# Kernel tuning notes

Measured on AMD Instinct MI355X. Metric: run time of the kernel, lower is better.

The kernel has to match this reference:

```python
import jax, jax.numpy as jnp
import numpy as np
from jax import lax

CONTEXT = 7
EPS = 1e-5  # BatchNorm2d default eps
DN = ('NCHW', 'OIHW', 'NCHW')


def _cbr(x, W, b, g, be, m, v, padding):
    # conv2d + BatchNorm (eval, running stats) + ReLU
    y = lax.conv_general_dilated(x, W, (1, 1), padding, dimension_numbers=DN)
    y = y + b[None, :, None, None]
    y = (y - m[None, :, None, None]) * (g / jnp.sqrt(v + EPS))[None, :, None, None] + be[None, :, None, None]
    return jax.nn.relu(y)


def _pool21(x):  # MaxPool2d(kernel_size=(2,1))
    return lax.reduce_window(x, -jnp.inf, lax.max, (1, 1, 2, 1), (1, 1, 2, 1), 'VALID')


def setup_inputs() -> dict:
    key = jax.random.key(0)
    ks = jax.random.split(key, 16)
    B, T, F, NC = 16, 108, 144, 25
    d = {}
    d['x'] = jax.random.normal(ks[0], (B, T, F), jnp.float32)
    d['labels'] = jax.random.randint(ks[1], (B, T), 0, NC)
    shapes = [(32, 1, 3, 3), (32, 32, 3, 3), (32, 32, 3, 3), (32, 32, 3, 3),
              (64, 32, 3, 3), (64, 64, 3, 3), (128, 64, 12, 9)]
    for i, s in enumerate(shapes, 1):
        fan_in = s[1] * s[2] * s[3]
        d[f'W{i}'] = jax.random.normal(ks[1 + i], s, jnp.float32) / np.sqrt(fan_in).astype(np.float32)
        c = s[0]
        d[f'b{i}'] = jnp.zeros((c,), jnp.float32)
        d[f'g{i}'] = jnp.ones((c,), jnp.float32)
        d[f'be{i}'] = jnp.zeros((c,), jnp.float32)
        d[f'm{i}'] = jnp.zeros((c,), jnp.float32)
        d[f'v{i}'] = jnp.ones((c,), jnp.float32)
    d['W8'] = jax.random.normal(ks[9], (NC, 128, 1, 1), jnp.float32) / np.float32(np.sqrt(128.0))
    d['b8'] = jnp.zeros((NC,), jnp.float32)
    return d


def reference(x, labels,
              W1, b1, g1, be1, m1, v1,
              W2, b2, g2, be2, m2, v2,
              W3, b3, g3, be3, m3, v3,
              W4, b4, g4, be4, m4, v4,
              W5, b5, g5, be5, m5, v5,
              W6, b6, g6, be6, m6, v6,
              W7, b7, g7, be7, m7, v7,
              W8, b8):
    B, T, F = x.shape
    win_len = 2 * CONTEXT + 1
    # permute to [B, F, T], zero-pad time by CONTEXT on both sides
    xp = jnp.pad(jnp.transpose(x, (0, 2, 1)), ((0, 0), (0, 0), (CONTEXT, CONTEXT)))
    # vectorized sliding windows (replaces the nested python loop of slices+cat)
    idx = jnp.arange(T)[:, None] + jnp.arange(win_len)[None, :]  # [T, 15]
    win = xp[:, :, idx]                                          # [B, F, T, 15]
    h = jnp.transpose(win, (0, 2, 1, 3)).reshape(B * T, 1, F, win_len)
    h = _cbr(h, W1, b1, g1, be1, m1, v1, 'SAME')
    h = _cbr(h, W2, b2, g2, be2, m2, v2, 'SAME')
    h = _cbr(h, W3, b3, g3, be3, m3, v3, 'SAME')
    h = _cbr(h, W4, b4, g4, be4, m4, v4, 'SAME')
    h = _pool21(h)  # dropout2d is identity in eval
    h = _cbr(h, W5, b5, g5, be5, m5, v5, 'VALID')
    h = _cbr(h, W6, b6, g6, be6, m6, v6, 'VALID')
    h = _pool21(h)
    h = _cbr(h, W7, b7, g7, be7, m7, v7, 'VALID')
    h = lax.conv_general_dilated(h, W8, (1, 1), 'VALID', dimension_numbers=DN) + b8[None, :, None, None]
    logits = jnp.mean(h, axis=(2, 3))  # AvgPool2d over full spatial extent
    return logits.reshape(B, T, -1)    # probs_out=True -> CRF input
```

## Files before the change

kernel.cpp:

```cpp
#include <hip/hip_runtime.h>
#include <hip/hip_bf16.h>
#include <hip/hip_fp16.h>

#define REGH 93440
#define C6N 26112

typedef _Float16 v8h __attribute__((ext_vector_type(8)));
typedef float v4f __attribute__((ext_vector_type(4)));
typedef unsigned short u16x8 __attribute__((ext_vector_type(8)));

__device__ inline float h2f(unsigned short u) {
    union { unsigned short s; _Float16 h; } v; v.s = u; return (float)v.h;
}
__device__ inline unsigned short f2h(float f) {
    union { unsigned short s; _Float16 h; } v; v.h = (_Float16)f; return v.s;
}

__global__ void repack_k(const float* __restrict__ W, const float* __restrict__ bb,
                         const float* __restrict__ gg, const float* __restrict__ be,
                         const float* __restrict__ mm, const float* __restrict__ vv,
                         float* __restrict__ wOut, float* __restrict__ tOut,
                         int CIN, int KHW, int COUT)
{
    int gid = blockIdx.x * 256 + threadIdx.x;
    if (gid < COUT) {
        float s = gg[gid] * rsqrtf(vv[gid] + 1e-5f);
        tOut[gid] = (bb[gid] - mm[gid]) * s + be[gid];
    }
    int tot = CIN * KHW * COUT;
    if (gid >= tot) return;
    int co = gid % COUT;
    int rest = gid / COUT;
    int k = rest % KHW;
    int ci = rest / KHW;
    float s = gg[co] * rsqrtf(vv[co] + 1e-5f);
    wOut[gid] = W[(co * CIN + ci) * KHW + k] * s;
}

__global__ void repack_mfma_k(const float* __restrict__ W, const float* __restrict__ bb,
                              const float* __restrict__ gg, const float* __restrict__ be,
                              const float* __restrict__ mm, const float* __restrict__ vv,
                              unsigned short* __restrict__ frag, float* __restrict__ tOut,
                              int CIN, int NT, int HALVES)
{
    int gid = blockIdx.x * 256 + threadIdx.x;
    int COUT = NT * 16;
    if (gid < COUT) {
        float s = gg[gid] * rsqrtf(vv[gid] + 1e-5f);
        tOut[gid] = (bb[gid] - mm[gid]) * s + be[gid];
    }
    int tot = 9 * HALVES * NT * 512;
    if (gid >= tot) return;
    int j    = gid & 7;
    int lane = (gid >> 3) & 63;
    int nt   = (gid >> 9) % NT;
    int rest = (gid >> 9) / NT;
    int half = rest % HALVES;
    int khw  = rest / HALVES;
    int ci   = half * 32 + (lane >> 4) * 8 + j;
    int co   = nt * 16 + (lane & 15);
    int kh   = khw / 3, kw = khw % 3;
    float s = gg[co] * rsqrtf(vv[co] + 1e-5f);
    frag[gid] = f2h(W[((co * CIN + ci) * 3 + kh) * 3 + kw] * s);
}

__global__ void repack7_k(const float* __restrict__ W, const float* __restrict__ bb,
                          const float* __restrict__ gg, const float* __restrict__ be,
                          const float* __restrict__ mm, const float* __restrict__ vv,
                          unsigned short* __restrict__ frag, float* __restrict__ tOut)
{
    int gid = blockIdx.x * 256 + threadIdx.x;
    if (gid < 128) {
        float s = gg[gid] * rsqrtf(vv[gid] + 1e-5f);
        tOut[gid] = (bb[gid] - mm[gid]) * s + be[gid];
    }
    if (gid >= 884736) return;
    int j    = gid & 7;
    int lane = (gid >> 3) & 63;
    int nt   = (gid >> 9) & 7;
    int half = (gid >> 12) & 1;
    int khw  = gid >> 13;
    int co   = nt * 16 + (lane & 15);
    int ci   = half * 32 + (lane >> 4) * 8 + j;
    int kh   = khw / 9, kw = khw - kh * 9;
    float s = gg[co] * rsqrtf(vv[co] + 1e-5f);
    frag[gid] = f2h(W[((co * 64 + ci) * 12 + kh) * 9 + kw] * s);
}

__global__ void zero_rings_k(unsigned short* __restrict__ bufA,
                             unsigned short* __restrict__ bufB, int cn)
{
    int gid = blockIdx.x * 256 + threadIdx.x;
    int tot = cn * 2 * 4 * 328;
    if (gid >= tot) return;
    int e = gid % 328;
    int rest = gid / 328;
    int cg = rest % 4; rest /= 4;
    int bsel = rest & 1;
    int nl = rest >> 1;
    unsigned short* base = (bsel ? bufB : bufA) + (size_t)nl * REGH + cg * 23360;
    int row, col;
    if (e < 40) { row = (e < 20) ? 0 : 145; col = (e < 20) ? e : e - 20; }
    else { int e2 = e - 40; row = 1 + (e2 >> 1); col = (e2 & 1) ? 16 : 0; }
    *(u16x8*)(base + (row * 20 + col) * 8) = (u16x8){0,0,0,0,0,0,0,0};
}

__global__ __launch_bounds__(256) void conv1_k(
    const float* __restrict__ x, unsigned short* __restrict__ out,
    const float* __restrict__ wr, const float* __restrict__ tv,
    int c0, int cn)
{
    int gid = blockIdx.x * 256 + threadIdx.x;
    if (gid >= cn * 2160) return;
    int nl = gid / 2160, p = gid - nl * 2160;
    int f = p / 15, w = p - f * 15;
    int n = c0 + nl;
    int b = n / 108, t = n - b * 108;

    float acc[32];
#pragma unroll
    for (int i = 0; i < 32; ++i) acc[i] = 0.f;

    for (int kh = 0; kh < 3; ++kh) {
        int ff = f + kh - 1;
        if (ff < 0 || ff >= 144) continue;
        for (int kw = 0; kw < 3; ++kw) {
            int c = w + kw - 1;
            if (c < 0 || c >= 15) continue;
            int tt = t + c - 7;
            if (tt < 0 || tt >= 108) continue;
            float xval = x[(b * 108 + tt) * 144 + ff];
            const float* wp = wr + (kh * 3 + kw) * 32;
#pragma unroll
            for (int q = 0; q < 8; ++q) {
                float4 wv = *(const float4*)(wp + q * 4);
                acc[q * 4 + 0] = fmaf(xval, wv.x, acc[q * 4 + 0]);
                acc[q * 4 + 1] = fmaf(xval, wv.y, acc[q * 4 + 1]);
                acc[q * 4 + 2] = fmaf(xval, wv.z, acc[q * 4 + 2]);
                acc[q * 4 + 3] = fmaf(xval, wv.w, acc[q * 4 + 3]);
            }
        }
    }
    unsigned short* ob = out + (size_t)nl * REGH + ((f + 1) * 20 + (w + 1)) * 8;
#pragma unroll
    for (int cg = 0; cg < 4; ++cg) {
        u16x8 pk;
#pragma unroll
        for (int c = 0; c < 8; ++c)
            pk[c] = f2h(fmaxf(acc[cg * 8 + c] + tv[cg * 8 + c], 0.f));
        *(u16x8*)(ob + cg * 23360) = pk;
    }
}

template<bool POOL>
__global__ __launch_bounds__(256) void conv234m_k(
    const unsigned short* __restrict__ in, unsigned short* __restrict__ out,
    const unsigned short* __restrict__ frag, const float* __restrict__ tv)
{
    __shared__ __align__(16) unsigned short sA[11552];
    const int band = blockIdx.x;
    const int n = blockIdx.y;
    const int tid = threadIdx.x;
    const int wave = tid >> 6, lane = tid & 63;
    const int m = lane & 15, quad = lane >> 4;

    {
        const float4* src = (const float4*)(in + (size_t)n * REGH);
        float4* dst = (float4*)sA;
        for (int i = tid; i < 1440; i += 256) {
            int q = i / 360, pos = i - q * 360;
            dst[q * 361 + pos] = src[q * 2920 + band * 320 + pos];
        }
    }
    __syncthreads();

    int mt[4], la0[4];
#pragma unroll
    for (int wt = 0; wt < 4; ++wt) {
        int t = wave * 4 + wt; if (t > 14) t = 14;
        mt[wt] = t;
        int p = band * 240 + t * 16 + m;
        int r, w;
        if (POOL) { int pr = p / 30, rem = p - pr * 30; w = rem >> 1; r = pr * 2 + (rem & 1); }
        else      { r = p / 15; w = p - r * 15; }
        la0[wt] = ((r - band * 16) * 20 + w) * 8;
    }

    v4f acc[2][4];
#pragma unroll
    for (int nt = 0; nt < 2; ++nt)
#pragma unroll
        for (int wt = 0; wt < 4; ++wt) acc[nt][wt] = (v4f){0.f,0.f,0.f,0.f};

    const unsigned short* sQ = sA + quad * 361 * 8;
#pragma unroll
    for (int khw = 0; khw < 9; ++khw) {
        const int shift = ((khw / 3) * 20 + (khw % 3)) * 8;
        v8h a[4];
#pragma unroll
        for (int wt = 0; wt < 4; ++wt)
            a[wt] = *(const v8h*)(sQ + la0[wt] + shift);
#pragma unroll
        for (int nt = 0; nt < 2; ++nt) {
            v8h b = *(const v8h*)(frag + (khw * 2 + nt) * 512 + lane * 8);
#pragma unroll
            for (int wt = 0; wt < 4; ++wt)
                acc[nt][wt] = __builtin_amdgcn_mfma_f32_16x16x32_f16(a[wt], b, acc[nt][wt], 0, 0, 0);
        }
    }

    unsigned short* outN = out + (size_t)n * REGH;
#pragma unroll
    for (int wt = 0; wt < 4; ++wt) {
        const int pb = band * 240 + mt[wt] * 16 + quad * 4;
#pragma unroll
        for (int nt = 0; nt < 2; ++nt) {
            const int co = nt * 16 + m;
            const float tb = tv[co];
            unsigned short* ob = outN + (co >> 3) * (POOL ? 9216 : 23360) + (co & 7);
            if (POOL) {
#pragma unroll
                for (int pi = 0; pi < 2; ++pi) {
                    int pe = pb + pi * 2;
                    int pr = pe / 30, rem = pe - pr * 30, w = rem >> 1;
                    float v0 = fmaxf(acc[nt][wt][pi * 2] + tb, 0.f);
                    float v1 = fmaxf(acc[nt][wt][pi * 2 + 1] + tb, 0.f);
                    ob[(pr * 16 + w) * 8] = f2h(fmaxf(v0, v1));
                }
            } else {
#pragma unroll
                for (int reg = 0; reg < 4; ++reg) {
                    int pr = pb + reg;
                    int f = pr / 15, w = pr - f * 15;
                    ob[((f + 1) * 20 + (w + 1)) * 8] = f2h(fmaxf(acc[nt][wt][reg] + tb, 0.f));
                }
            }
        }
    }
}

__global__ __launch_bounds__(256) void conv5m_k(
    const unsigned short* __restrict__ in, unsigned short* __restrict__ out,
    const unsigned short* __restrict__ frag, const float* __restrict__ tv)
{
    const int n = blockIdx.y;
    const int tid = threadIdx.x;
    const int wave = tid >> 6, lane = tid & 63;
    const int m = lane & 15, quad = lane >> 4;
    const unsigned short* inN = in + (size_t)n * REGH + quad * 9216;

    int mt[2], a0[2];
#pragma unroll
    for (int wt = 0; wt < 2; ++wt) {
        int t = blockIdx.x * 8 + wave * 2 + wt; if (t > 56) t = 56;
        mt[wt] = t;
        int p = t * 16 + m; if (p > 909) p = 909;
        int r = p / 13, w = p - r * 13;
        a0[wt] = (r * 16 + w) * 8;
    }

    v4f acc[4][2];
#pragma unroll
    for (int nt = 0; nt < 4; ++nt)
#pragma unroll
        for (int wt = 0; wt < 2; ++wt) acc[nt][wt] = (v4f){0.f,0.f,0.f,0.f};

#pragma unroll
    for (int khw = 0; khw < 9; ++khw) {
        const int shift = ((khw / 3) * 16 + (khw % 3)) * 8;
        v8h a[2];
#pragma unroll
        for (int wt = 0; wt < 2; ++wt)
            a[wt] = *(const v8h*)(inN + a0[wt] + shift);
#pragma unroll
        for (int nt = 0; nt < 4; ++nt) {
            v8h b = *(const v8h*)(frag + (khw * 4 + nt) * 512 + lane * 8);
#pragma unroll
            for (int wt = 0; wt < 2; ++wt)
                acc[nt][wt] = __builtin_amdgcn_mfma_f32_16x16x32_f16(a[wt], b, acc[nt][wt], 0, 0, 0);
        }
    }

    unsigned short* outN = out + (size_t)n * REGH;
#pragma unroll
    for (int wt = 0; wt < 2; ++wt) {
        const int pb = mt[wt] * 16 + quad * 4;
#pragma unroll
        for (int nt = 0; nt < 4; ++nt) {
            const int co = nt * 16 + m;
            const float tb = tv[co];
            unsigned short* ob = outN + (co >> 3) * 8960 + (co & 7);
#pragma unroll
            for (int reg = 0; reg < 4; ++reg) {
                int p = pb + reg;
                if (p < 910) {
                    int r = p / 13, w = p - r * 13;
                    ob[(r * 16 + w) * 8] = f2h(fmaxf(acc[nt][wt][reg] + tb, 0.f));
                }
            }
        }
    }
}

__global__ __launch_bounds__(256) void conv6m_k(
    const unsigned short* __restrict__ in, unsigned short* __restrict__ c6,
    const unsigned short* __restrict__ frag, const float* __restrict__ tv)
{
    const int n = blockIdx.y;
    const int tid = threadIdx.x;
    const int wave = tid >> 6, lane = tid & 63;
    const int m = lane & 15, quad = lane >> 4;
    const unsigned short* inN = in + (size_t)n * REGH;

    int mt[2], a0[2];
#pragma unroll
    for (int wt = 0; wt < 2; ++wt) {
        int t = blockIdx.x * 8 + wave * 2 + wt; if (t > 46) t = 46;
        mt[wt] = t;
        int p = t * 16 + m; if (p > 747) p = 747;
        int pr = p / 22, rem = p - pr * 22;
        int w = rem >> 1, r = pr * 2 + (rem & 1);
        a0[wt] = (r * 16 + w) * 8;
    }

    v4f acc[4][2];
#pragma unroll
    for (int nt = 0; nt < 4; ++nt)
#pragma unroll
        for (int wt = 0; wt < 2; ++wt) acc[nt][wt] = (v4f){0.f,0.f,0.f,0.f};

#pragma unroll
    for (int khw = 0; khw < 9; ++khw) {
        const int shift = ((khw / 3) * 16 + (khw % 3)) * 8;
#pragma unroll
        for (int half = 0; half < 2; ++half) {
            const unsigned short* ip = inN + (half * 4 + quad) * 8960 + shift;
            v8h a[2];
#pragma unroll
            for (int wt = 0; wt < 2; ++wt)
                a[wt] = *(const v8h*)(ip + a0[wt]);
#pragma unroll
            for (int nt = 0; nt < 4; ++nt) {
                v8h b = *(const v8h*)(frag + ((khw * 2 + half) * 4 + nt) * 512 + lane * 8);
#pragma unroll
                for (int wt = 0; wt < 2; ++wt)
                    acc[nt][wt] = __builtin_amdgcn_mfma_f32_16x16x32_f16(a[wt], b, acc[nt][wt], 0, 0, 0);
            }
        }
    }

    unsigned short* outN = c6 + (size_t)n * C6N;
#pragma unroll
    for (int wt = 0; wt < 2; ++wt) {
        const int pb = mt[wt] * 16 + quad * 4;
#pragma unroll
        for (int nt = 0; nt < 4; ++nt) {
            const int co = nt * 16 + m;
            const float tb = tv[co];
            unsigned short* ob = outN + (co >> 3) * 3264 + (co & 7);
#pragma unroll
            for (int pi = 0; pi < 2; ++pi) {
                int pe = pb + pi * 2;
                if (pe < 748) {
                    int pr = pe / 22, rem = pe - pr * 22, w = rem >> 1;
                    float v0 = fmaxf(acc[nt][wt][pi * 2] + tb, 0.f);
                    float v1 = fmaxf(acc[nt][wt][pi * 2 + 1] + tb, 0.f);
                    ob[(pr * 12 + w) * 8] = f2h(fmaxf(v0, v1));
                }
            }
        }
    }
}

__global__ __launch_bounds__(256) void conv7mfma_k(
    const unsigned short* __restrict__ c6, float* __restrict__ pooled,
    const unsigned short* __restrict__ frag7, const float* __restrict__ tv)
{
    __shared__ __align__(16) unsigned short sA[14176];
    const int n = blockIdx.x;
    const int tid = threadIdx.x;
    const int wave = tid >> 6;
    const int lane = tid & 63;
    const int m = lane & 15;
    const int quad = lane >> 4;

    int pm[5];
#pragma unroll
    for (int mt = 0; mt < 5; ++mt) {
        int p = mt * 16 + m;
        if (p >= 69) p = 0;
        pm[mt] = (p / 3) * 13 + (p % 3);
    }

    v4f acc[2][5];
#pragma unroll
    for (int t = 0; t < 2; ++t)
#pragma unroll
        for (int mt = 0; mt < 5; ++mt)
            acc[t][mt] = (v4f){0.f, 0.f, 0.f, 0.f};

    for (int half = 0; half < 2; ++half) {
        __syncthreads();
        {
            const float4* src = (const float4*)(c6 + (size_t)n * C6N + half * 13056);
            float4* dst = (float4*)sA;
            for (int i = tid; i < 1632; i += 256) {
                int q = i / 408, pos = i - q * 408;
                int h = pos / 12, w = pos - h * 12;
                dst[q * 443 + h * 13 + w] = src[i];
            }
        }
        __syncthreads();
        for (int khw = 0; khw < 108; ++khw) {
            const int off = (khw / 9) * 13 + (khw % 9);
            v8h a[5];
#pragma unroll
            for (int mt = 0; mt < 5; ++mt)
                a[mt] = *(const v8h*)(sA + (quad * 443 + pm[mt] + off) * 8);
            const unsigned short* bp = frag7
                + ((size_t)(khw * 2 + half) * 8) * 512 + lane * 8;
#pragma unroll
            for (int t = 0; t < 2; ++t) {
                const int nt = wave + t * 4;
                v8h b = *(const v8h*)(bp + nt * 512);
#pragma unroll
                for (int mt = 0; mt < 5; ++mt)
                    acc[t][mt] = __builtin_amdgcn_mfma_f32_16x16x32_f16(
                        a[mt], b, acc[t][mt], 0, 0, 0);
            }
        }
    }

    float s[2] = {0.f, 0.f};
#pragma unroll
    for (int t = 0; t < 2; ++t) {
        const float tb = tv[(wave + t * 4) * 16 + m];
#pragma unroll
        for (int mt = 0; mt < 5; ++mt) {
#pragma unroll
            for (int rr = 0; rr < 4; ++rr) {
                int p = mt * 16 + quad * 4 + rr;
                if (p < 69) s[t] += fmaxf(acc[t][mt][rr] + tb, 0.f);
            }
        }
    }
#pragma unroll
    for (int t = 0; t < 2; ++t) {
        s[t] += __shfl_xor(s[t], 16);
        s[t] += __shfl_xor(s[t], 32);
    }
    if (lane < 16) {
#pragma unroll
        for (int t = 0; t < 2; ++t)
            pooled[(size_t)n * 128 + (wave + t * 4) * 16 + lane] = s[t] * (1.f / 69.f);
    }
}

__global__ void logits_k(const float* __restrict__ pooled, const float* __restrict__ W8,
                         const float* __restrict__ b8, float* __restrict__ outg,
                         int total)
{
    int gid = blockIdx.x * 256 + threadIdx.x;
    if (gid >= total * 25) return;
    int nl = gid / 25, c = gid - nl * 25;
    const float* pp = pooled + (size_t)nl * 128;
    const float* wp = W8 + c * 128;
    float s = b8[c];
#pragma unroll
    for (int ci = 0; ci < 128; ci += 4) {
        float4 wv = *(const float4*)(wp + ci);
        float4 pv = *(const float4*)(pp + ci);
        s = fmaf(wv.x, pv.x, s);
        s = fmaf(wv.y, pv.y, s);
        s = fmaf(wv.z, pv.z, s);
        s = fmaf(wv.w, pv.w, s);
    }
    outg[(size_t)nl * 25 + c] = s;
}

extern "C" void kernel_launch(void* const* d_in, const int* in_sizes, int n_in,
                              void* d_out, int out_size, void* d_ws, size_t ws_size,
                              hipStream_t stream)
{
    const float* x = (const float*)d_in[0];
    const float* Wl[8]; const float* bl[8]; const float* gl[8];
    const float* bel[8]; const float* ml[8]; const float* vl[8];
    for (int i = 1; i <= 7; ++i) {
        int o = 2 + (i - 1) * 6;
        Wl[i]  = (const float*)d_in[o + 0];
        bl[i]  = (const float*)d_in[o + 1];
        gl[i]  = (const float*)d_in[o + 2];
        bel[i] = (const float*)d_in[o + 3];
        ml[i]  = (const float*)d_in[o + 4];
        vl[i]  = (const float*)d_in[o + 5];
    }
    const float* W8 = (const float*)d_in[44];
    const float* b8 = (const float*)d_in[45];
    float* ws = (float*)d_ws;

    float* wr1 = ws + 0;        float* t1 = ws + 288;
    unsigned short* f2b = (unsigned short*)(ws + 320);
    float* t2 = ws + 4928;
    unsigned short* f3b = (unsigned short*)(ws + 4960);
    float* t3 = ws + 9568;
    unsigned short* f4b = (unsigned short*)(ws + 9600);
    float* t4 = ws + 14208;
    unsigned short* f5b = (unsigned short*)(ws + 14240);
    float* t5 = ws + 23456;
    unsigned short* f6b = (unsigned short*)(ws + 23520);
    float* t6 = ws + 41952;
    unsigned short* f7b = (unsigned short*)(ws + 42016);
    float* t7 = ws + 484384;
    const size_t WFL = 484512;

    unsigned short* c6buf = (unsigned short*)(ws + WFL);
    const size_t C6FL = (size_t)1728 * C6N / 2;
    float* pooled = ws + WFL + C6FL;
    const size_t FIXED = WFL + C6FL + (size_t)1728 * 128;

    size_t avail_fl = ws_size / 4;
    size_t buf_halves = (avail_fl > FIXED) ? (avail_fl - FIXED) * 2 : 0;
    int Cs = (int)(buf_halves / (2 * (size_t)REGH));
    if (Cs < 1) Cs = 1;
    if (Cs > 1728) Cs = 1728;
    unsigned short* bufA = (unsigned short*)(ws + FIXED);
    unsigned short* bufB = bufA + (size_t)Cs * REGH;

    auto g1 = [](int t) { return (t + 255) / 256; };

    repack_k<<<g1(288), 256, 0, stream>>>(Wl[1], bl[1], gl[1], bel[1], ml[1], vl[1], wr1, t1, 1, 9, 32);
    repack_mfma_k<<<g1(9216),  256, 0, stream>>>(Wl[2], bl[2], gl[2], bel[2], ml[2], vl[2], f2b, t2, 32, 2, 1);
    repack_mfma_k<<<g1(9216),  256, 0, stream>>>(Wl[3], bl[3], gl[3], bel[3], ml[3], vl[3], f3b, t3, 32, 2, 1);
    repack_mfma_k<<<g1(9216),  256, 0, stream>>>(Wl[4], bl[4], gl[4], bel[4], ml[4], vl[4], f4b, t4, 32, 2, 1);
    repack_mfma_k<<<g1(18432), 256, 0, stream>>>(Wl[5], bl[5], gl[5], bel[5], ml[5], vl[5], f5b, t5, 32, 4, 1);
    repack_mfma_k<<<g1(36864), 256, 0, stream>>>(Wl[6], bl[6], gl[6], bel[6], ml[6], vl[6], f6b, t6, 64, 4, 2);
    repack7_k<<<g1(884736), 256, 0, stream>>>(Wl[7], bl[7], gl[7], bel[7], ml[7], vl[7], f7b, t7);

    for (int c0 = 0; c0 < 1728; c0 += Cs) {
        int cn = (1728 - c0 < Cs) ? (1728 - c0) : Cs;
        zero_rings_k<<<g1(cn * 2624), 256, 0, stream>>>(bufA, bufB, cn);
        conv1_k<<<g1(cn * 2160), 256, 0, stream>>>(x, bufA, wr1, t1, c0, cn);
        conv234m_k<false><<<dim3(9, cn), 256, 0, stream>>>(bufA, bufB, f2b, t2);
        conv234m_k<false><<<dim3(9, cn), 256, 0, stream>>>(bufB, bufA, f3b, t3);
        conv234m_k<true ><<<dim3(9, cn), 256, 0, stream>>>(bufA, bufB, f4b, t4);
        conv5m_k<<<dim3(8, cn), 256, 0, stream>>>(bufB, bufA, f5b, t5);
        conv6m_k<<<dim3(6, cn), 256, 0, stream>>>(bufA, c6buf + (size_t)c0 * C6N, f6b, t6);
    }

    conv7mfma_k<<<1728, 256, 0, stream>>>(c6buf, pooled, f7b, t7);
    logits_k<<<g1(1728 * 25), 256, 0, stream>>>(pooled, W8, b8, (float*)d_out, 1728);
}
```

Measured before the change: 1.379 ms.

## Split conv7 K-loop across wave pairs and hoist ring zeroing out of chunk loop

conv7mfma_k now gives each wave 4 N-tiles and half of the 108 kernel positions, instead of 2 N-tiles over all positions. The two K-halves are combined through shared memory before bias, ReLU and the average. This lets each A fragment feed twice as many MFMAs, cutting LDS reads per MFMA, at the cost of more accumulator registers (80 floats) and a shared-memory reduction. It also zeroes the buffer rings once before the chunk loop rather than on every chunk, which assumes later kernels never overwrite the rings.

Result: slower. 1.472 ms (+6.8%).

```diff
diff --git a/kernel.cpp b/kernel.cpp
--- a/kernel.cpp
+++ b/kernel.cpp
@@ -376,13 +376,17 @@
     const unsigned short* __restrict__ c6, float* __restrict__ pooled,
     const unsigned short* __restrict__ frag7, const float* __restrict__ tv)
 {
-    __shared__ __align__(16) unsigned short sA[14176];
+    __shared__ __align__(16) unsigned char smem[40960];
+    unsigned short* sA = (unsigned short*)smem;
+    float* sC = (float*)smem;
     const int n = blockIdx.x;
     const int tid = threadIdx.x;
     const int wave = tid >> 6;
     const int lane = tid & 63;
     const int m = lane & 15;
     const int quad = lane >> 4;
+    const int ks = wave >> 1;
+    const int ns = wave & 1;
 
     int pm[5];
 #pragma unroll
@@ -392,9 +396,9 @@
         pm[mt] = (p / 3) * 13 + (p % 3);
     }
 
-    v4f acc[2][5];
-#pragma unroll
-    for (int t = 0; t < 2; ++t)
+    v4f acc[4][5];
+#pragma unroll
+    for (int t = 0; t < 4; ++t)
 #pragma unroll
         for (int mt = 0; mt < 5; ++mt)
             acc[t][mt] = (v4f){0.f, 0.f, 0.f, 0.f};
@@ -411,18 +415,18 @@
             }
         }
         __syncthreads();
-        for (int khw = 0; khw < 108; ++khw) {
+        for (int kk = 0; kk < 54; ++kk) {
+            const int khw = ks * 54 + kk;
             const int off = (khw / 9) * 13 + (khw % 9);
             v8h a[5];
 #pragma unroll
             for (int mt = 0; mt < 5; ++mt)
                 a[mt] = *(const v8h*)(sA + (quad * 443 + pm[mt] + off) * 8);
             const unsigned short* bp = frag7
-                + ((size_t)(khw * 2 + half) * 8) * 512 + lane * 8;
-#pragma unroll
-            for (int t = 0; t < 2; ++t) {
-                const int nt = wave + t * 4;
-                v8h b = *(const v8h*)(bp + nt * 512);
+                + ((size_t)((khw * 2 + half) * 8 + ns * 4)) * 512 + lane * 8;
+#pragma unroll
+            for (int t = 0; t < 4; ++t) {
+                v8h b = *(const v8h*)(bp + t * 512);
 #pragma unroll
                 for (int mt = 0; mt < 5; ++mt)
                     acc[t][mt] = __builtin_amdgcn_mfma_f32_16x16x32_f16(
@@ -431,28 +435,40 @@
         }
     }
 
-    float s[2] = {0.f, 0.f};
-#pragma unroll
-    for (int t = 0; t < 2; ++t) {
-        const float tb = tv[(wave + t * 4) * 16 + m];
-#pragma unroll
-        for (int mt = 0; mt < 5; ++mt) {
-#pragma unroll
-            for (int rr = 0; rr < 4; ++rr) {
-                int p = mt * 16 + quad * 4 + rr;
-                if (p < 69) s[t] += fmaxf(acc[t][mt][rr] + tb, 0.f);
-            }
-        }
-    }
-#pragma unroll
-    for (int t = 0; t < 2; ++t) {
-        s[t] += __shfl_xor(s[t], 16);
-        s[t] += __shfl_xor(s[t], 32);
-    }
-    if (lane < 16) {
-#pragma unroll
-        for (int t = 0; t < 2; ++t)
-            pooled[(size_t)n * 128 + (wave + t * 4) * 16 + lane] = s[t] * (1.f / 69.f);
+    __syncthreads();
+    if (ks == 1) {
+#pragma unroll
+        for (int t = 0; t < 4; ++t)
+#pragma unroll
+            for (int mt = 0; mt < 5; ++mt)
+                *(v4f*)(sC + (((ns * 20) + t * 5 + mt) * 64 + lane) * 4) = acc[t][mt];
+    }
+    __syncthreads();
+    if (ks == 0) {
+        float s[4] = {0.f, 0.f, 0.f, 0.f};
+#pragma unroll
+        for (int t = 0; t < 4; ++t) {
+            const float tb = tv[ns * 64 + t * 16 + m];
+#pragma unroll
+            for (int mt = 0; mt < 5; ++mt) {
+                v4f pc = *(const v4f*)(sC + (((ns * 20) + t * 5 + mt) * 64 + lane) * 4);
+#pragma unroll
+                for (int rr = 0; rr < 4; ++rr) {
+                    int p = mt * 16 + quad * 4 + rr;
+                    if (p < 69) s[t] += fmaxf(acc[t][mt][rr] + pc[rr] + tb, 0.f);
+                }
+            }
+        }
+#pragma unroll
+        for (int t = 0; t < 4; ++t) {
+            s[t] += __shfl_xor(s[t], 16);
+            s[t] += __shfl_xor(s[t], 32);
+        }
+        if (lane < 16) {
+#pragma unroll
+            for (int t = 0; t < 4; ++t)
+                pooled[(size_t)n * 128 + ns * 64 + t * 16 + lane] = s[t] * (1.f / 69.f);
+        }
     }
 }
 
@@ -536,9 +552,10 @@
     repack_mfma_k<<<g1(36864), 256, 0, stream>>>(Wl[6], bl[6], gl[6], bel[6], ml[6], vl[6], f6b, t6, 64, 4, 2);
     repack7_k<<<g1(884736), 256, 0, stream>>>(Wl[7], bl[7], gl[7], bel[7], ml[7], vl[7], f7b, t7);
 
+    zero_rings_k<<<g1(Cs * 2624), 256, 0, stream>>>(bufA, bufB, Cs);
+
     for (int c0 = 0; c0 < 1728; c0 += Cs) {
         int cn = (1728 - c0 < Cs) ? (1728 - c0) : Cs;
-        zero_rings_k<<<g1(cn * 2624), 256, 0, stream>>>(bufA, bufB, cn);
         conv1_k<<<g1(cn * 2160), 256, 0, stream>>>(x, bufA, wr1, t1, c0, cn);
         conv234m_k<false><<<dim3(9, cn), 256, 0, stream>>>(bufA, bufB, f2b, t2);
         conv234m_k<false><<<dim3(9, cn), 256, 0, stream>>>(bufB, bufA, f3b, t3);
```

## Tighten activation row stride, hoist ring zeroing, fuse logits into conv7

Applied to the files above, without the earlier changes.

The padded activation row stride drops from 20 to 17 pixels. This shrinks the per-sample buffer, the LDS tile in the conv2-4 kernels and the global traffic per band. Ring zeroing moves out of the chunk loop and runs once, and the 1x1 logits conv plus bias is folded into the conv7 epilogue through a small shared array, which removes a kernel launch and the pooled intermediate. Zeroing the rings only once is correct only if later layers never overwrite those ring cells. The pooled layouts of conv4 and conv5 write into the same buffers, so with several chunks the rings could hold stale data.

Result: faster. 1.350 ms (-2.0%).

```diff
diff --git a/kernel.cpp b/kernel.cpp
--- a/kernel.cpp
+++ b/kernel.cpp
@@ -2,7 +2,8 @@
 #include <hip/hip_bf16.h>
 #include <hip/hip_fp16.h>
 
-#define REGH 93440
+#define REGH 79424
+#define CGS1 19856
 #define C6N 26112
 
 typedef _Float16 v8h __attribute__((ext_vector_type(8)));
@@ -91,18 +92,18 @@
                              unsigned short* __restrict__ bufB, int cn)
 {
     int gid = blockIdx.x * 256 + threadIdx.x;
-    int tot = cn * 2 * 4 * 328;
+    int tot = cn * 2 * 4 * 322;
     if (gid >= tot) return;
-    int e = gid % 328;
-    int rest = gid / 328;
+    int e = gid % 322;
+    int rest = gid / 322;
     int cg = rest % 4; rest /= 4;
     int bsel = rest & 1;
     int nl = rest >> 1;
-    unsigned short* base = (bsel ? bufB : bufA) + (size_t)nl * REGH + cg * 23360;
+    unsigned short* base = (bsel ? bufB : bufA) + (size_t)nl * REGH + cg * CGS1;
     int row, col;
-    if (e < 40) { row = (e < 20) ? 0 : 145; col = (e < 20) ? e : e - 20; }
-    else { int e2 = e - 40; row = 1 + (e2 >> 1); col = (e2 & 1) ? 16 : 0; }
-    *(u16x8*)(base + (row * 20 + col) * 8) = (u16x8){0,0,0,0,0,0,0,0};
+    if (e < 34) { row = (e < 17) ? 0 : 145; col = (e < 17) ? e : e - 17; }
+    else { int e2 = e - 34; row = 1 + (e2 >> 1); col = (e2 & 1) ? 16 : 0; }
+    *(u16x8*)(base + (row * 17 + col) * 8) = (u16x8){0,0,0,0,0,0,0,0};
 }
 
 __global__ __launch_bounds__(256) void conv1_k(
@@ -141,14 +142,14 @@
             }
         }
     }
-    unsigned short* ob = out + (size_t)nl * REGH + ((f + 1) * 20 + (w + 1)) * 8;
+    unsigned short* ob = out + (size_t)nl * REGH + ((f + 1) * 17 + (w + 1)) * 8;
 #pragma unroll
     for (int cg = 0; cg < 4; ++cg) {
         u16x8 pk;
 #pragma unroll
         for (int c = 0; c < 8; ++c)
             pk[c] = f2h(fmaxf(acc[cg * 8 + c] + tv[cg * 8 + c], 0.f));
-        *(u16x8*)(ob + cg * 23360) = pk;
+        *(u16x8*)(ob + cg * CGS1) = pk;
     }
 }
 
@@ -157,7 +158,7 @@
     const unsigned short* __restrict__ in, unsigned short* __restrict__ out,
     const unsigned short* __restrict__ frag, const float* __restrict__ tv)
 {
-    __shared__ __align__(16) unsigned short sA[11552];
+    __shared__ __align__(16) unsigned short sA[9824];
     const int band = blockIdx.x;
     const int n = blockIdx.y;
     const int tid = threadIdx.x;
@@ -167,9 +168,9 @@
     {
         const float4* src = (const float4*)(in + (size_t)n * REGH);
         float4* dst = (float4*)sA;
-        for (int i = tid; i < 1440; i += 256) {
-            int q = i / 360, pos = i - q * 360;
-            dst[q * 361 + pos] = src[q * 2920 + band * 320 + pos];
+        for (int i = tid; i < 1224; i += 256) {
+            int q = i / 306, pos = i - q * 306;
+            dst[q * 307 + pos] = src[q * 2482 + band * 272 + pos];
         }
     }
     __syncthreads();
@@ -183,7 +184,7 @@
         int r, w;
         if (POOL) { int pr = p / 30, rem = p - pr * 30; w = rem >> 1; r = pr * 2 + (rem & 1); }
         else      { r = p / 15; w = p - r * 15; }
-        la0[wt] = ((r - band * 16) * 20 + w) * 8;
+        la0[wt] = ((r - band * 16) * 17 + w) * 8;
     }
 
     v4f acc[2][4];
@@ -192,10 +193,10 @@
 #pragma unroll
         for (int wt = 0; wt < 4; ++wt) acc[nt][wt] = (v4f){0.f,0.f,0.f,0.f};
 
-    const unsigned short* sQ = sA + quad * 361 * 8;
+    const unsigned short* sQ = sA + quad * 307 * 8;
 #pragma unroll
     for (int khw = 0; khw < 9; ++khw) {
-        const int shift = ((khw / 3) * 20 + (khw % 3)) * 8;
+        const int shift = ((khw / 3) * 17 + (khw % 3)) * 8;
         v8h a[4];
 #pragma unroll
         for (int wt = 0; wt < 4; ++wt)
@@ -217,7 +218,7 @@
         for (int nt = 0; nt < 2; ++nt) {
             const int co = nt * 16 + m;
             const float tb = tv[co];
-            unsigned short* ob = outN + (co >> 3) * (POOL ? 9216 : 23360) + (co & 7);
+            unsigned short* ob = outN + (co >> 3) * (POOL ? 9216 : CGS1) + (co & 7);
             if (POOL) {
 #pragma unroll
                 for (int pi = 0; pi < 2; ++pi) {
@@ -232,7 +233,7 @@
                 for (int reg = 0; reg < 4; ++reg) {
                     int pr = pb + reg;
                     int f = pr / 15, w = pr - f * 15;
-                    ob[((f + 1) * 20 + (w + 1)) * 8] = f2h(fmaxf(acc[nt][wt][reg] + tb, 0.f));
+                    ob[((f + 1) * 17 + (w + 1)) * 8] = f2h(fmaxf(acc[nt][wt][reg] + tb, 0.f));
                 }
             }
         }
@@ -373,10 +374,12 @@
 }
 
 __global__ __launch_bounds__(256) void conv7mfma_k(
-    const unsigned short* __restrict__ c6, float* __restrict__ pooled,
-    const unsigned short* __restrict__ frag7, const float* __restrict__ tv)
+    const unsigned short* __restrict__ c6, float* __restrict__ outg,
+    const unsigned short* __restrict__ frag7, const float* __restrict__ tv,
+    const float* __restrict__ W8, const float* __restrict__ b8)
 {
     __shared__ __align__(16) unsigned short sA[14176];
+    __shared__ float sP[128];
     const int n = blockIdx.x;
     const int tid = threadIdx.x;
     const int wave = tid >> 6;
@@ -452,30 +455,23 @@
     if (lane < 16) {
 #pragma unroll
         for (int t = 0; t < 2; ++t)
-            pooled[(size_t)n * 128 + (wave + t * 4) * 16 + lane] = s[t] * (1.f / 69.f);
-    }
-}
-
-__global__ void logits_k(const float* __restrict__ pooled, const float* __restrict__ W8,
-                         const float* __restrict__ b8, float* __restrict__ outg,
-                         int total)
-{
-    int gid = blockIdx.x * 256 + threadIdx.x;
-    if (gid >= total * 25) return;
-    int nl = gid / 25, c = gid - nl * 25;
-    const float* pp = pooled + (size_t)nl * 128;
-    const float* wp = W8 + c * 128;
-    float s = b8[c];
-#pragma unroll
-    for (int ci = 0; ci < 128; ci += 4) {
-        float4 wv = *(const float4*)(wp + ci);
-        float4 pv = *(const float4*)(pp + ci);
-        s = fmaf(wv.x, pv.x, s);
-        s = fmaf(wv.y, pv.y, s);
-        s = fmaf(wv.z, pv.z, s);
-        s = fmaf(wv.w, pv.w, s);
-    }
-    outg[(size_t)nl * 25 + c] = s;
+            sP[(wave + t * 4) * 16 + lane] = s[t] * (1.f / 69.f);
+    }
+    __syncthreads();
+
+    if (tid < 25) {
+        const float* wp = W8 + tid * 128;
+        float sc = b8[tid];
+#pragma unroll
+        for (int ci = 0; ci < 128; ci += 4) {
+            float4 wv = *(const float4*)(wp + ci);
+            sc = fmaf(wv.x, sP[ci],     sc);
+            sc = fmaf(wv.y, sP[ci + 1], sc);
+            sc = fmaf(wv.z, sP[ci + 2], sc);
+            sc = fmaf(wv.w, sP[ci + 3], sc);
+        }
+        outg[(size_t)n * 25 + tid] = sc;
+    }
 }
 
 extern "C" void kernel_launch(void* const* d_in, const int* in_sizes, int n_in,
@@ -515,8 +511,7 @@
 
     unsigned short* c6buf = (unsigned short*)(ws + WFL);
     const size_t C6FL = (size_t)1728 * C6N / 2;
-    float* pooled = ws + WFL + C6FL;
-    const size_t FIXED = WFL + C6FL + (size_t)1728 * 128;
+    const size_t FIXED = WFL + C6FL;
 
     size_t avail_fl = ws_size / 4;
     size_t buf_halves = (avail_fl > FIXED) ? (avail_fl - FIXED) * 2 : 0;
@@ -536,9 +531,10 @@
     repack_mfma_k<<<g1(36864), 256, 0, stream>>>(Wl[6], bl[6], gl[6], bel[6], ml[6], vl[6], f6b, t6, 64, 4, 2);
     repack7_k<<<g1(884736), 256, 0, stream>>>(Wl[7], bl[7], gl[7], bel[7], ml[7], vl[7], f7b, t7);
 
+    zero_rings_k<<<g1(Cs * 2576), 256, 0, stream>>>(bufA, bufB, Cs);
+
     for (int c0 = 0; c0 < 1728; c0 += Cs) {
         int cn = (1728 - c0 < Cs) ? (1728 - c0) : Cs;
-        zero_rings_k<<<g1(cn * 2624), 256, 0, stream>>>(bufA, bufB, cn);
         conv1_k<<<g1(cn * 2160), 256, 0, stream>>>(x, bufA, wr1, t1, c0, cn);
         conv234m_k<false><<<dim3(9, cn), 256, 0, stream>>>(bufA, bufB, f2b, t2);
         conv234m_k<false><<<dim3(9, cn), 256, 0, stream>>>(bufB, bufA, f3b, t3);
@@ -547,6 +543,5 @@
         conv6m_k<<<dim3(6, cn), 256, 0, stream>>>(bufA, c6buf + (size_t)c0 * C6N, f6b, t6);
     }
 
-    conv7mfma_k<<<1728, 256, 0, stream>>>(c6buf, pooled, f7b, t7);
-    logits_k<<<g1(1728 * 25), 256, 0, stream>>>(pooled, W8, b8, (float*)d_out, 1728);
-}
+    conv7mfma_k<<<1728, 256, 0, stream>>>(c6buf, (float*)d_out, f7b, t7, W8, b8);
+}
```

## Drop padded activation rings and interleave ping-pong buffers per sample

Applied to the files above, without the earlier changes.

Activation buffers now hold unpadded 144x15 planes, and the conv2-4 kernels synthesize the zero halo while staging into shared memory. This removes the separate ring-zeroing kernel and cuts the bytes stored and read per sample. BufA and bufB are now interleaved inside one per-sample slot (offset TA), so both ping-pong halves of a sample sit close together in memory. The cost is extra bounds checks and index math in the shared-memory load loop.

New measurement: 1.170 ms. 1.18x faster.

```diff
diff --git a/kernel.cpp b/kernel.cpp
--- a/kernel.cpp
+++ b/kernel.cpp
@@ -2,7 +2,9 @@
 #include <hip/hip_bf16.h>
 #include <hip/hip_fp16.h>
 
-#define REGH 93440
+#define TA 71680
+#define TB 69120
+#define SLOT 140800
 #define C6N 26112
 
 typedef _Float16 v8h __attribute__((ext_vector_type(8)));
@@ -87,24 +89,6 @@
     frag[gid] = f2h(W[((co * 64 + ci) * 12 + kh) * 9 + kw] * s);
 }
 
-__global__ void zero_rings_k(unsigned short* __restrict__ bufA,
-                             unsigned short* __restrict__ bufB, int cn)
-{
-    int gid = blockIdx.x * 256 + threadIdx.x;
-    int tot = cn * 2 * 4 * 328;
-    if (gid >= tot) return;
-    int e = gid % 328;
-    int rest = gid / 328;
-    int cg = rest % 4; rest /= 4;
-    int bsel = rest & 1;
-    int nl = rest >> 1;
-    unsigned short* base = (bsel ? bufB : bufA) + (size_t)nl * REGH + cg * 23360;
-    int row, col;
-    if (e < 40) { row = (e < 20) ? 0 : 145; col = (e < 20) ? e : e - 20; }
-    else { int e2 = e - 40; row = 1 + (e2 >> 1); col = (e2 & 1) ? 16 : 0; }
-    *(u16x8*)(base + (row * 20 + col) * 8) = (u16x8){0,0,0,0,0,0,0,0};
-}
-
 __global__ __launch_bounds__(256) void conv1_k(
     const float* __restrict__ x, unsigned short* __restrict__ out,
     const float* __restrict__ wr, const float* __restrict__ tv,
@@ -141,14 +125,14 @@
             }
         }
     }
-    unsigned short* ob = out + (size_t)nl * REGH + ((f + 1) * 20 + (w + 1)) * 8;
+    unsigned short* ob = out + (size_t)nl * SLOT + (f * 15 + w) * 8;
 #pragma unroll
     for (int cg = 0; cg < 4; ++cg) {
         u16x8 pk;
 #pragma unroll
         for (int c = 0; c < 8; ++c)
             pk[c] = f2h(fmaxf(acc[cg * 8 + c] + tv[cg * 8 + c], 0.f));
-        *(u16x8*)(ob + cg * 23360) = pk;
+        *(u16x8*)(ob + cg * 17280) = pk;
     }
 }
 
@@ -157,7 +141,7 @@
     const unsigned short* __restrict__ in, unsigned short* __restrict__ out,
     const unsigned short* __restrict__ frag, const float* __restrict__ tv)
 {
-    __shared__ __align__(16) unsigned short sA[11552];
+    __shared__ __align__(16) unsigned short sA[9824];
     const int band = blockIdx.x;
     const int n = blockIdx.y;
     const int tid = threadIdx.x;
@@ -165,11 +149,17 @@
     const int m = lane & 15, quad = lane >> 4;
 
     {
-        const float4* src = (const float4*)(in + (size_t)n * REGH);
+        const float4* src = (const float4*)(in + (size_t)n * SLOT);
         float4* dst = (float4*)sA;
-        for (int i = tid; i < 1440; i += 256) {
-            int q = i / 360, pos = i - q * 360;
-            dst[q * 361 + pos] = src[q * 2920 + band * 320 + pos];
+        for (int i = tid; i < 1224; i += 256) {
+            int q = i / 306, pos = i - q * 306;
+            int r = pos / 17, c = pos - r * 17;
+            int ir = band * 16 + r - 1;
+            int ic = c - 1;
+            float4 v = {0.f, 0.f, 0.f, 0.f};
+            if (ir >= 0 && ir < 144 && ic >= 0 && ic < 15)
+                v = src[q * 2160 + ir * 15 + ic];
+            dst[q * 307 + pos] = v;
         }
     }
     __syncthreads();
@@ -183,7 +173,7 @@
         int r, w;
         if (POOL) { int pr = p / 30, rem = p - pr * 30; w = rem >> 1; r = pr * 2 + (rem & 1); }
         else      { r = p / 15; w = p - r * 15; }
-        la0[wt] = ((r - band * 16) * 20 + w) * 8;
+        la0[wt] = ((r - band * 16) * 17 + w) * 8;
     }
 
     v4f acc[2][4];
@@ -192,10 +182,10 @@
 #pragma unroll
         for (int wt = 0; wt < 4; ++wt) acc[nt][wt] = (v4f){0.f,0.f,0.f,0.f};
 
-    const unsigned short* sQ = sA + quad * 361 * 8;
+    const unsigned short* sQ = sA + quad * 307 * 8;
 #pragma unroll
     for (int khw = 0; khw < 9; ++khw) {
-        const int shift = ((khw / 3) * 20 + (khw % 3)) * 8;
+        const int shift = ((khw / 3) * 17 + (khw % 3)) * 8;
         v8h a[4];
 #pragma unroll
         for (int wt = 0; wt < 4; ++wt)
@@ -209,7 +199,7 @@
         }
     }
 
-    unsigned short* outN = out + (size_t)n * REGH;
+    unsigned short* outN = out + (size_t)n * SLOT;
 #pragma unroll
     for (int wt = 0; wt < 4; ++wt) {
         const int pb = band * 240 + mt[wt] * 16 + quad * 4;
@@ -217,7 +207,7 @@
         for (int nt = 0; nt < 2; ++nt) {
             const int co = nt * 16 + m;
             const float tb = tv[co];
-            unsigned short* ob = outN + (co >> 3) * (POOL ? 9216 : 23360) + (co & 7);
+            unsigned short* ob = outN + (co >> 3) * (POOL ? 9216 : 17280) + (co & 7);
             if (POOL) {
 #pragma unroll
                 for (int pi = 0; pi < 2; ++pi) {
@@ -232,7 +222,7 @@
                 for (int reg = 0; reg < 4; ++reg) {
                     int pr = pb + reg;
                     int f = pr / 15, w = pr - f * 15;
-                    ob[((f + 1) * 20 + (w + 1)) * 8] = f2h(fmaxf(acc[nt][wt][reg] + tb, 0.f));
+                    ob[(f * 15 + w) * 8] = f2h(fmaxf(acc[nt][wt][reg] + tb, 0.f));
                 }
             }
         }
@@ -247,7 +237,7 @@
     const int tid = threadIdx.x;
     const int wave = tid >> 6, lane = tid & 63;
     const int m = lane & 15, quad = lane >> 4;
-    const unsigned short* inN = in + (size_t)n * REGH + quad * 9216;
+    const unsigned short* inN = in + (size_t)n * SLOT + quad * 9216;
 
     int mt[2], a0[2];
 #pragma unroll
@@ -281,7 +271,7 @@
         }
     }
 
-    unsigned short* outN = out + (size_t)n * REGH;
+    unsigned short* outN = out + (size_t)n * SLOT;
 #pragma unroll
     for (int wt = 0; wt < 2; ++wt) {
         const int pb = mt[wt] * 16 + quad * 4;
@@ -310,7 +300,7 @@
     const int tid = threadIdx.x;
     const int wave = tid >> 6, lane = tid & 63;
     const int m = lane & 15, quad = lane >> 4;
-    const unsigned short* inN = in + (size_t)n * REGH;
+    const unsigned short* inN = in + (size_t)n * SLOT;
 
     int mt[2], a0[2];
 #pragma unroll
@@ -520,11 +510,11 @@
 
     size_t avail_fl = ws_size / 4;
     size_t buf_halves = (avail_fl > FIXED) ? (avail_fl - FIXED) * 2 : 0;
-    int Cs = (int)(buf_halves / (2 * (size_t)REGH));
+    int Cs = (int)(buf_halves / (size_t)SLOT);
     if (Cs < 1) Cs = 1;
     if (Cs > 1728) Cs = 1728;
     unsigned short* bufA = (unsigned short*)(ws + FIXED);
-    unsigned short* bufB = bufA + (size_t)Cs * REGH;
+    unsigned short* bufB = bufA + TA;
 
     auto g1 = [](int t) { return (t + 255) / 256; };
 
@@ -538,7 +528,6 @@
 
     for (int c0 = 0; c0 < 1728; c0 += Cs) {
         int cn = (1728 - c0 < Cs) ? (1728 - c0) : Cs;
-        zero_rings_k<<<g1(cn * 2624), 256, 0, stream>>>(bufA, bufB, cn);
         conv1_k<<<g1(cn * 2160), 256, 0, stream>>>(x, bufA, wr1, t1, c0, cn);
         conv234m_k<false><<<dim3(9, cn), 256, 0, stream>>>(bufA, bufB, f2b, t2);
         conv234m_k<false><<<dim3(9, cn), 256, 0, stream>>>(bufB, bufA, f3b, t3);
```
